# Optimization experiments

Measured on AMD Instinct MI355X. Metric: run time of the kernel, lower is better.

## Reference

```python
import jax, jax.numpy as jnp
import numpy as np

HEADS = 16
NEG = -1.0e9


def setup_inputs() -> dict:
    key = jax.random.key(0)
    ks = jax.random.split(key, 9)
    B, T, E = 2, 2048, 1024
    s = 1.0 / np.sqrt(E)
    return {
        "x": jax.random.normal(ks[0], (B, T, E), dtype=jnp.float32),
        "Wq": jax.random.normal(ks[1], (E, E), dtype=jnp.float32) * s,
        "bq": jax.random.normal(ks[2], (E,), dtype=jnp.float32) * 0.01,
        "Wk": jax.random.normal(ks[3], (E, E), dtype=jnp.float32) * s,
        "bk": jax.random.normal(ks[4], (E,), dtype=jnp.float32) * 0.01,
        "Wv": jax.random.normal(ks[5], (E, E), dtype=jnp.float32) * s,
        "bv": jax.random.normal(ks[6], (E,), dtype=jnp.float32) * 0.01,
        "Wo": jax.random.normal(ks[7], (E, E), dtype=jnp.float32) * s,
        "bo": jax.random.normal(ks[8], (E,), dtype=jnp.float32) * 0.01,
    }


def reference(x, Wq, bq, Wk, bk, Wv, bv, Wo, bo):
    B, T, E = x.shape
    H = HEADS
    D = E // H
    # In the original forward (idx_t=-2, context=None): context = x, so
    # values(x), keys(context), queries(context) all read x.
    v = (x @ Wv + bv).reshape(B, T, H, D)
    k = (x @ Wk + bk).reshape(B, T, H, D)
    q = (x @ Wq + bq).reshape(B, T, H, D)
    # causal mask: 1 above diagonal, 0 on/below; broadcast over (B, H)
    mask = 1.0 - jnp.tril(jnp.ones((T, T), dtype=x.dtype))  # [T, T]
    energy = jnp.einsum("bqhd,bkhd->bhqk", q, k)
    # Faithful to source: mask*(-1e9) added BEFORE the sqrt(embed_size) scaling
    energy = energy + mask[None, None] * jnp.asarray(NEG, dtype=x.dtype)
    attn = jax.nn.softmax(energy / jnp.sqrt(jnp.asarray(E, dtype=x.dtype)), axis=-1)
    out = jnp.einsum("bhqk,bkhd->bqhd", attn, v).reshape(B, T, E)
    return out @ Wo + bo
```

## Files before the change

### kernel.cpp

```cpp
#include <hip/hip_runtime.h>
#include <hip/hip_bf16.h>
#include <stdint.h>


typedef __attribute__((ext_vector_type(8))) short short8;
typedef __attribute__((ext_vector_type(4))) short short4v;
typedef __attribute__((ext_vector_type(4))) float f32x4;

#define MFMA16(a, b, c) __builtin_amdgcn_mfma_f32_16x16x32_bf16((a), (b), (c), 0, 0, 0)

static __device__ __forceinline__ unsigned short f2bf(float f) {
    union { float f; unsigned int u; } v; v.f = f;
    unsigned int r = v.u + 0x7fffu + ((v.u >> 16) & 1u);
    return (unsigned short)(r >> 16);
}

static __device__ __forceinline__ void gld16(const unsigned short* g,
                                             unsigned short* l) {
    __builtin_amdgcn_global_load_lds(
        (const __attribute__((address_space(1))) unsigned int*)g,
        (__attribute__((address_space(3))) unsigned int*)l, 16, 0, 0);
}

__global__ __launch_bounds__(256) void k_convert_x(const float* __restrict__ x,
                                                   unsigned short* __restrict__ xb) {
    int i = blockIdx.x * 256 + threadIdx.x;
    const float4* p = (const float4*)(x + (size_t)i * 8);
    float4 a = p[0], b = p[1];
    short8 o;
    o[0] = (short)f2bf(a.x); o[1] = (short)f2bf(a.y);
    o[2] = (short)f2bf(a.z); o[3] = (short)f2bf(a.w);
    o[4] = (short)f2bf(b.x); o[5] = (short)f2bf(b.y);
    o[6] = (short)f2bf(b.z); o[7] = (short)f2bf(b.w);
    ((short8*)xb)[i] = o;
}

__global__ __launch_bounds__(256) void k_transpose_w4(
        const float* __restrict__ W0, const float* __restrict__ W1,
        const float* __restrict__ W2, const float* __restrict__ W3,
        unsigned short* __restrict__ T0, unsigned short* __restrict__ T1,
        unsigned short* __restrict__ T2, unsigned short* __restrict__ T3) {
    const float* W = (blockIdx.z == 0) ? W0 : (blockIdx.z == 1) ? W1
                     : (blockIdx.z == 2) ? W2 : W3;
    unsigned short* Wt = (blockIdx.z == 0) ? T0 : (blockIdx.z == 1) ? T1
                         : (blockIdx.z == 2) ? T2 : T3;
    __shared__ float tw[64][68];
    const int k0 = blockIdx.x * 64, n0 = blockIdx.y * 64;
    const int tid = threadIdx.x;
#pragma unroll
    for (int r = 0; r < 4; ++r) {
        int i = tid + r * 256;
        int row = i >> 4, c4 = (i & 15) * 4;
        float4 v = *(const float4*)(W + (size_t)(k0 + row) * 1024 + n0 + c4);
        *(float4*)(&tw[row][c4]) = v;
    }
    __syncthreads();
#pragma unroll
    for (int r = 0; r < 2; ++r) {
        int i = tid + r * 256;
        int nrow = i >> 3, kc = (i & 7) * 8;
        short8 o;
#pragma unroll
        for (int j = 0; j < 8; ++j) o[j] = (short)f2bf(tw[kc + j][nrow]);
        *(short8*)(Wt + (size_t)(n0 + nrow) * 1024 + k0 + kc) = o;
    }
}

template <int MODE>
__global__ __launch_bounds__(256) void k_gemm2(const unsigned short* __restrict__ A,
                                               const unsigned short* __restrict__ Bt,
                                               const float* __restrict__ bq,
                                               const float* __restrict__ bk,
                                               const float* __restrict__ bv,
                                               unsigned short* __restrict__ Qb,
                                               unsigned short* __restrict__ Kb,
                                               unsigned short* __restrict__ Vt,
                                               float* __restrict__ Co) {
    const int tid = threadIdx.x;
    const int w = tid >> 6, lane = tid & 63;
    const int quad = lane >> 4, l16 = lane & 15;
    const int wm = w >> 1, wn = w & 1;
    const int m0 = blockIdx.x * 128, n0 = blockIdx.y * 128;
    const int lrow = lane >> 2, lch = (lane & 3) * 8;

    const unsigned short* ga = A + (size_t)(m0 + w * 32 + lrow) * 1024 + lch;
    const unsigned short* gb = Bt + (size_t)(n0 + w * 32 + lrow) * 1024 + lch;
    const int lofs = w * 1024 + lane * 8;

    f32x4 acc[4][4];
#pragma unroll
    for (int mt = 0; mt < 4; ++mt)
#pragma unroll
        for (int nt = 0; nt < 4; ++nt) acc[mt][nt] = (f32x4){0.f, 0.f, 0.f, 0.f};

    if constexpr (MODE == 0) {
        __shared__ unsigned short As[128 * 32];
        __shared__ unsigned short Bs[128 * 32];
        for (int k0 = 0; k0 < 1024; k0 += 32) {
            __syncthreads();
            gld16(ga + k0, &As[lofs]);
            gld16(ga + 16 * 1024 + k0, &As[lofs + 512]);
            gld16(gb + k0, &Bs[lofs]);
            gld16(gb + 16 * 1024 + k0, &Bs[lofs + 512]);
            __syncthreads();
            short8 af[4], bf[4];
#pragma unroll
            for (int mt = 0; mt < 4; ++mt)
                af[mt] = *(const short8*)(&As[(wm * 64 + mt * 16 + l16) * 32 + quad * 8]);
#pragma unroll
            for (int nt = 0; nt < 4; ++nt)
                bf[nt] = *(const short8*)(&Bs[(wn * 64 + nt * 16 + l16) * 32 + quad * 8]);
#pragma unroll
            for (int mt = 0; mt < 4; ++mt)
#pragma unroll
                for (int nt = 0; nt < 4; ++nt)
                    acc[mt][nt] = MFMA16(af[mt], bf[nt], acc[mt][nt]);
        }
    } else {
        __shared__ unsigned short As[2][128 * 32];
        __shared__ unsigned short Bs[2][128 * 32];
        short8 ar0 = *(const short8*)(ga);
        short8 ar1 = *(const short8*)(ga + 16 * 1024);
        short8 br0 = *(const short8*)(gb);
        short8 br1 = *(const short8*)(gb + 16 * 1024);
        *(short8*)(&As[0][lofs]) = ar0;
        *(short8*)(&As[0][lofs + 512]) = ar1;
        *(short8*)(&Bs[0][lofs]) = br0;
        *(short8*)(&Bs[0][lofs + 512]) = br1;
        __syncthreads();

        for (int k0 = 0; k0 < 1024; k0 += 32) {
            const int cur = (k0 >> 5) & 1;
            const bool more = (k0 + 32) < 1024;
            if (more) {
                ar0 = *(const short8*)(ga + k0 + 32);
                ar1 = *(const short8*)(ga + 16 * 1024 + k0 + 32);
                br0 = *(const short8*)(gb + k0 + 32);
                br1 = *(const short8*)(gb + 16 * 1024 + k0 + 32);
            }
            short8 af[4], bf[4];
#pragma unroll
            for (int mt = 0; mt < 4; ++mt)
                af[mt] = *(const short8*)(&As[cur][(wm * 64 + mt * 16 + l16) * 32 + quad * 8]);
#pragma unroll
            for (int nt = 0; nt < 4; ++nt)
                bf[nt] = *(const short8*)(&Bs[cur][(wn * 64 + nt * 16 + l16) * 32 + quad * 8]);
#pragma unroll
            for (int mt = 0; mt < 4; ++mt)
#pragma unroll
                for (int nt = 0; nt < 4; ++nt)
                    acc[mt][nt] = MFMA16(af[mt], bf[nt], acc[mt][nt]);
            if (more) {
                const int nxt = cur ^ 1;
                *(short8*)(&As[nxt][lofs]) = ar0;
                *(short8*)(&As[nxt][lofs + 512]) = ar1;
                *(short8*)(&Bs[nxt][lofs]) = br0;
                *(short8*)(&Bs[nxt][lofs + 512]) = br1;
                __syncthreads();
            }
        }
    }

    if (MODE == 1) {
#pragma unroll
        for (int nt = 0; nt < 4; ++nt) {
            int col = n0 + wn * 64 + nt * 16 + l16;
            float bb = bq[col];
#pragma unroll
            for (int mt = 0; mt < 4; ++mt) {
                int row = m0 + wm * 64 + mt * 16 + quad * 4;
#pragma unroll
                for (int r = 0; r < 4; ++r)
                    Co[(size_t)(row + r) * 1024 + col] = acc[mt][nt][r] + bb;
            }
        }
    } else if (n0 < 2048) {
        unsigned short* C = (n0 < 1024) ? Qb : Kb;
        const float* bias = (n0 < 1024) ? bq : bk;
        const float sc = (n0 < 1024) ? 0.03125f : 1.0f;
        int cb = (n0 < 1024) ? n0 : (n0 - 1024);
#pragma unroll
        for (int nt = 0; nt < 4; ++nt) {
            int col = cb + wn * 64 + nt * 16 + l16;
            float bb = bias[col];
#pragma unroll
            for (int mt = 0; mt < 4; ++mt) {
                int row = m0 + wm * 64 + mt * 16 + quad * 4;
#pragma unroll
                for (int r = 0; r < 4; ++r)
                    C[(size_t)(row + r) * 1024 + col] = f2bf((acc[mt][nt][r] + bb) * sc);
            }
        }
    } else {
#pragma unroll
        for (int nt = 0; nt < 4; ++nt) {
            int vcol = (n0 - 2048) + wn * 64 + nt * 16 + l16;
            float bb = bv[vcol];
#pragma unroll
            for (int mt = 0; mt < 4; ++mt) {
                int row = m0 + wm * 64 + mt * 16 + quad * 4;
                int b = row >> 11, t = row & 2047;
                short4v o;
#pragma unroll
                for (int r = 0; r < 4; ++r) o[r] = (short)f2bf(acc[mt][nt][r] + bb);
                *(short4v*)(&Vt[((size_t)(b * 16 + (vcol >> 6)) * 64 + (vcol & 63))
                                    * 2048 + t]) = o;
            }
        }
    }
}

__global__ __launch_bounds__(256) void k_attn(const unsigned short* __restrict__ Qb,
                                              const unsigned short* __restrict__ Kb,
                                              const unsigned short* __restrict__ Vt,
                                              unsigned short* __restrict__ Ob) {
    __shared__ unsigned short Ks[2][64][72];
    __shared__ unsigned short Vs[2][64][72];
    __shared__ unsigned short Ps[4][16][72];
    const int tid = threadIdx.x;
    const int w = tid >> 6, lane = tid & 63;
    const int quad = lane >> 4, l16 = lane & 15;
    const int id = blockIdx.x;
    const int bh = (id & 7) + 8 * ((id >> 3) & 3);
    const int qb = 31 - (id >> 5);
    const int b = bh >> 4, h = bh & 15;
    const int qg = qb * 64 + w * 16 + l16;
    const f32x4 zero4 = {0.f, 0.f, 0.f, 0.f};

    const int srow = tid >> 3, sc8 = (tid & 7) * 8;
    const unsigned short* kg0 = Kb + (size_t)(b * 2048) * 1024 + h * 64 + sc8;
    const unsigned short* vg0 = Vt + (size_t)(bh * 64 + srow) * 2048 + sc8;

    short8 qf[2];
    {
        const unsigned short* qp =
            Qb + (size_t)(b * 2048 + qg) * 1024 + h * 64 + quad * 8;
        qf[0] = *(const short8*)(qp);
        qf[1] = *(const short8*)(qp + 32);
    }
    float m_ = -1e30f, l_ = 0.f;
    f32x4 o[4];
#pragma unroll
    for (int dt = 0; dt < 4; ++dt) o[dt] = zero4;

    short8 kr0, kr1, vr0, vr1;
    kr0 = *(const short8*)(kg0 + (size_t)(srow) * 1024);
    kr1 = *(const short8*)(kg0 + (size_t)(32 + srow) * 1024);
    vr0 = *(const short8*)(vg0);
    vr1 = *(const short8*)(vg0 + (size_t)32 * 2048);
    *(short8*)(&Ks[0][srow][sc8]) = kr0;
    *(short8*)(&Ks[0][32 + srow][sc8]) = kr1;
    *(short8*)(&Vs[0][srow][sc8]) = vr0;
    *(short8*)(&Vs[0][32 + srow][sc8]) = vr1;
    __syncthreads();

    for (int kt = 0; kt <= qb; ++kt) {
        const int cur = kt & 1;
        const bool more = kt < qb;
        if (more) {
            const unsigned short* kg = kg0 + (size_t)((kt + 1) * 64) * 1024;
            kr0 = *(const short8*)(kg + (size_t)(srow) * 1024);
            kr1 = *(const short8*)(kg + (size_t)(32 + srow) * 1024);
            vr0 = *(const short8*)(vg0 + (kt + 1) * 64);
            vr1 = *(const short8*)(vg0 + (size_t)32 * 2048 + (kt + 1) * 64);
        }

        f32x4 s[4];
#pragma unroll
        for (int kkt = 0; kkt < 4; ++kkt) {
            short8 kf0 = *(const short8*)(&Ks[cur][kkt * 16 + l16][quad * 8]);
            short8 kf1 = *(const short8*)(&Ks[cur][kkt * 16 + l16][32 + quad * 8]);
            s[kkt] = MFMA16(kf0, qf[0], zero4);
            s[kkt] = MFMA16(kf1, qf[1], s[kkt]);
        }

        if (kt == qb) {
#pragma unroll
            for (int kkt = 0; kkt < 4; ++kkt) {
                int kg_ = qb * 64 + kkt * 16 + quad * 4;
#pragma unroll
                for (int r = 0; r < 4; ++r)
                    if (kg_ + r > qg) s[kkt][r] = -1e30f;
            }
        }
        float mx = -1e30f;
#pragma unroll
        for (int kkt = 0; kkt < 4; ++kkt)
#pragma unroll
            for (int r = 0; r < 4; ++r) mx = fmaxf(mx, s[kkt][r]);
        mx = fmaxf(mx, __shfl_xor(mx, 16, 64));
        mx = fmaxf(mx, __shfl_xor(mx, 32, 64));
        const float mold = m_;
        m_ = fmaxf(m_, mx);
        float sum = 0.f;
#pragma unroll
        for (int kkt = 0; kkt < 4; ++kkt)
#pragma unroll
            for (int r = 0; r < 4; ++r) {
                float p = __expf(s[kkt][r] - m_);
                s[kkt][r] = p;
                sum += p;
            }
        sum += __shfl_xor(sum, 16, 64);
        sum += __shfl_xor(sum, 32, 64);
        if (__any(m_ > mold)) {
            float al = __expf(mold - m_);
            l_ = l_ * al + sum;
#pragma unroll
            for (int dt = 0; dt < 4; ++dt)
#pragma unroll
                for (int r = 0; r < 4; ++r) o[dt][r] *= al;
        } else {
            l_ += sum;
        }

#pragma unroll
        for (int kkt = 0; kkt < 4; ++kkt) {
            short4v pk;
#pragma unroll
            for (int r = 0; r < 4; ++r) pk[r] = (short)f2bf(s[kkt][r]);
            *(short4v*)(&Ps[w][l16][kkt * 16 + quad * 4]) = pk;
        }
        __threadfence_block();

#pragma unroll
        for (int kks = 0; kks < 2; ++kks) {
            short8 pf = *(const short8*)(&Ps[w][l16][kks * 32 + quad * 8]);
#pragma unroll
            for (int dt = 0; dt < 4; ++dt) {
                short8 vf = *(const short8*)(
                    &Vs[cur][dt * 16 + l16][kks * 32 + quad * 8]);
                o[dt] = MFMA16(vf, pf, o[dt]);
            }
        }

        if (more) {
            const int nxt = cur ^ 1;
            *(short8*)(&Ks[nxt][srow][sc8]) = kr0;
            *(short8*)(&Ks[nxt][32 + srow][sc8]) = kr1;
            *(short8*)(&Vs[nxt][srow][sc8]) = vr0;
            *(short8*)(&Vs[nxt][32 + srow][sc8]) = vr1;
            __syncthreads();
        }
    }

    float inv = 1.0f / l_;
    unsigned short* op = Ob + (size_t)(b * 2048 + qg) * 1024 + h * 64 + quad * 4;
#pragma unroll
    for (int dt = 0; dt < 4; ++dt) {
        short4v ov;
#pragma unroll
        for (int r = 0; r < 4; ++r) ov[r] = (short)f2bf(o[dt][r] * inv);
        *(short4v*)(op + dt * 16) = ov;
    }
}

extern "C" void kernel_launch(void* const* d_in, const int* in_sizes, int n_in,
                              void* d_out, int out_size, void* d_ws, size_t ws_size,
                              hipStream_t stream) {
    const float* x  = (const float*)d_in[0];
    const float* Wq = (const float*)d_in[1];
    const float* bq = (const float*)d_in[2];
    const float* Wk = (const float*)d_in[3];
    const float* bk = (const float*)d_in[4];
    const float* Wv = (const float*)d_in[5];
    const float* bv = (const float*)d_in[6];
    const float* Wo = (const float*)d_in[7];
    const float* bo = (const float*)d_in[8];
    float* out = (float*)d_out;

    const size_t M4 = 4194304, M1 = 1048576;
    const size_t NEED = (M4 + M4 + 3 * M1 + M1) * 2;
    if (ws_size < NEED) return;
    unsigned short* ws = (unsigned short*)d_ws;
    unsigned short* xb  = ws;
    unsigned short* Ob  = ws;
    unsigned short* Vt  = ws + M4;
    unsigned short* WtQ = ws + 2 * M4;
    unsigned short* Wto = WtQ + 3 * M1;
    unsigned short* Qb  = (unsigned short*)d_out;
    unsigned short* Kb  = Qb + M4;

    k_convert_x<<<2048, 256, 0, stream>>>(x, xb);
    k_transpose_w4<<<dim3(16, 16, 4), 256, 0, stream>>>(
        Wq, Wk, Wv, Wo, WtQ, WtQ + M1, WtQ + 2 * M1, Wto);
    k_gemm2<0><<<dim3(32, 24), 256, 0, stream>>>(xb, WtQ, bq, bk, bv,
                                                 Qb, Kb, Vt, nullptr);
    k_attn<<<1024, 256, 0, stream>>>(Qb, Kb, Vt, Ob);
    k_gemm2<1><<<dim3(32, 8), 256, 0, stream>>>(Ob, Wto, bo, nullptr, nullptr,
                                                nullptr, nullptr, nullptr, out);
}
```

Before: 208.6 us.

## Single-buffer K/V tiles in attention and interleave causal block order

Shrinks the K/V shared-memory staging from double to single buffering, with an extra barrier before overwriting the tile. The aim is to lower LDS use per block so more blocks fit per CU. It also remaps block IDs to query blocks in a zigzag pattern (long, medium, short rows interleaved) to balance causal work across waves of blocks. The cost is one more __syncthreads per iteration and less overlap between loading the next tile and computing on the current one.

```diff
diff --git a/kernel.cpp b/kernel.cpp
--- a/kernel.cpp
+++ b/kernel.cpp
@@ -214,15 +214,17 @@
                                               const unsigned short* __restrict__ Kb,
                                               const unsigned short* __restrict__ Vt,
                                               unsigned short* __restrict__ Ob) {
-    __shared__ unsigned short Ks[2][64][72];
-    __shared__ unsigned short Vs[2][64][72];
+    __shared__ unsigned short Ks[64][72];
+    __shared__ unsigned short Vs[64][72];
     __shared__ unsigned short Ps[4][16][72];
     const int tid = threadIdx.x;
     const int w = tid >> 6, lane = tid & 63;
     const int quad = lane >> 4, l16 = lane & 15;
     const int id = blockIdx.x;
     const int bh = (id & 7) + 8 * ((id >> 3) & 3);
-    const int qb = 31 - (id >> 5);
+    const int g = id >> 5, gk = g & 7, gb2 = g >> 3;
+    const int qb = (gb2 == 0) ? 31 - gk : (gb2 == 1) ? 16 + gk
+                   : (gb2 == 2) ? 15 - gk : gk;
     const int b = bh >> 4, h = bh & 15;
     const int qg = qb * 64 + w * 16 + l16;
     const f32x4 zero4 = {0.f, 0.f, 0.f, 0.f};
@@ -248,14 +250,13 @@
     kr1 = *(const short8*)(kg0 + (size_t)(32 + srow) * 1024);
     vr0 = *(const short8*)(vg0);
     vr1 = *(const short8*)(vg0 + (size_t)32 * 2048);
-    *(short8*)(&Ks[0][srow][sc8]) = kr0;
-    *(short8*)(&Ks[0][32 + srow][sc8]) = kr1;
-    *(short8*)(&Vs[0][srow][sc8]) = vr0;
-    *(short8*)(&Vs[0][32 + srow][sc8]) = vr1;
+    *(short8*)(&Ks[srow][sc8]) = kr0;
+    *(short8*)(&Ks[32 + srow][sc8]) = kr1;
+    *(short8*)(&Vs[srow][sc8]) = vr0;
+    *(short8*)(&Vs[32 + srow][sc8]) = vr1;
     __syncthreads();
 
     for (int kt = 0; kt <= qb; ++kt) {
-        const int cur = kt & 1;
         const bool more = kt < qb;
         if (more) {
             const unsigned short* kg = kg0 + (size_t)((kt + 1) * 64) * 1024;
@@ -268,8 +269,8 @@
         f32x4 s[4];
 #pragma unroll
         for (int kkt = 0; kkt < 4; ++kkt) {
-            short8 kf0 = *(const short8*)(&Ks[cur][kkt * 16 + l16][quad * 8]);
-            short8 kf1 = *(const short8*)(&Ks[cur][kkt * 16 + l16][32 + quad * 8]);
+            short8 kf0 = *(const short8*)(&Ks[kkt * 16 + l16][quad * 8]);
+            short8 kf1 = *(const short8*)(&Ks[kkt * 16 + l16][32 + quad * 8]);
             s[kkt] = MFMA16(kf0, qf[0], zero4);
             s[kkt] = MFMA16(kf1, qf[1], s[kkt]);
         }
@@ -329,17 +330,17 @@
 #pragma unroll
             for (int dt = 0; dt < 4; ++dt) {
                 short8 vf = *(const short8*)(
-                    &Vs[cur][dt * 16 + l16][kks * 32 + quad * 8]);
+                    &Vs[dt * 16 + l16][kks * 32 + quad * 8]);
                 o[dt] = MFMA16(vf, pf, o[dt]);
             }
         }
 
         if (more) {
-            const int nxt = cur ^ 1;
-            *(short8*)(&Ks[nxt][srow][sc8]) = kr0;
-            *(short8*)(&Ks[nxt][32 + srow][sc8]) = kr1;
-            *(short8*)(&Vs[nxt][srow][sc8]) = vr0;
-            *(short8*)(&Vs[nxt][32 + srow][sc8]) = vr1;
+            __syncthreads();
+            *(short8*)(&Ks[srow][sc8]) = kr0;
+            *(short8*)(&Ks[32 + srow][sc8]) = kr1;
+            *(short8*)(&Vs[srow][sc8]) = vr0;
+            *(short8*)(&Vs[32 + srow][sc8]) = vr1;
             __syncthreads();
         }
     }
```

Result: faster. 197.2 us (-5.5%).
